# Kernel optimization log

Measured on AMD Instinct MI355X. Metric: run time of the kernel, lower is better.

The kernel has to match this reference:

```python
import math
import jax, jax.numpy as jnp
import numpy as np

B, D, K = 512, 512, 93431
S_SCALE = 64.0
MARGIN = 0.5
EPS = 0.1
COS_M = math.cos(MARGIN)
SIN_M = math.sin(MARGIN)
THRESHOLD = math.cos(math.pi - MARGIN)
MM = math.sin(math.pi - MARGIN) * MARGIN


def setup_inputs() -> dict:
    key = jax.random.key(0)
    k1, k2, k3 = jax.random.split(key, 3)
    x = jax.random.normal(k1, (B, D), dtype=jnp.float32)
    label = jax.random.randint(k2, (B,), 0, K, dtype=jnp.int64)
    kernel = jax.random.normal(k3, (D, K), dtype=jnp.float32) * 0.01
    t = jnp.zeros((1,), dtype=jnp.float32)
    return {"x": x, "label": label, "kernel": kernel, "t": t}


def reference(x, label, kernel, t):
    # L2-normalize embeddings (rows) and kernel (columns), cosine logits
    xn = x / jnp.linalg.norm(x, axis=1, keepdims=True)
    kn = kernel / jnp.linalg.norm(kernel, axis=0, keepdims=True)
    cos_theta = jnp.clip(xn @ kn, -1.0, 1.0)  # [B, K]

    rows = jnp.arange(B)
    target_logit = cos_theta[rows, label]  # [B]
    sin_theta = jnp.sqrt(1.0 - target_logit ** 2)
    cos_theta_m = target_logit * COS_M - sin_theta * SIN_M  # [B]

    mask = cos_theta > cos_theta_m[:, None]  # [B, K]
    final_target_logit = jnp.where(target_logit > THRESHOLD,
                                   cos_theta_m, target_logit - MM)

    # buffer update runs under no_grad in torch; updated t is used immediately
    t_new = jax.lax.stop_gradient(target_logit.mean() * 0.01 + 0.99 * t[0])

    # hard-example re-weighting, then scatter margin logit at the label column
    ct = jnp.where(mask, cos_theta * (t_new + cos_theta), cos_theta)
    ct = ct.at[rows, label].set(final_target_logit)
    logits = ct * S_SCALE

    # label-smoothed cross-entropy without materializing the one-hot matrix
    logp = jax.nn.log_softmax(logits, axis=1)  # [B, K]
    nll = (1.0 - EPS) * logp[rows, label] + (EPS / K) * logp.sum(axis=1)
    loss = -nll.mean()
    return loss
```

## Files before the change

### kernel.cpp

```cpp
#include <hip/hip_runtime.h>
#include <math.h>

#define BB 512
#define DD 512
#define KK 93431
#define KPAD 93440

#define S_SCALEf 64.0f
#define COS_Mf   0.87758256189037276f
#define SIN_Mf   0.47942553860420301f
#define THRESHf (-0.87758256189037276f)
#define MMf      0.23971276930210151f
#define EPSf     0.1f
#define MFIXf    65.0f

#define KSCALE 64.0f
#define XSCALE 16.0f
#define INV_KX (1.0f / (KSCALE * XSCALE))

typedef float f32x4 __attribute__((ext_vector_type(4)));
typedef long  l64x2 __attribute__((ext_vector_type(2)));

__device__ __forceinline__ unsigned pack4_fp8(float a, float b, float c, float d) {
    unsigned v = 0;
    v = __builtin_amdgcn_cvt_pk_fp8_f32(a, b, v, false);
    v = __builtin_amdgcn_cvt_pk_fp8_f32(c, d, v, true);
    return v;
}

__device__ __forceinline__ void gload16(const void* g, void* l) {
    __builtin_amdgcn_global_load_lds(
        (const __attribute__((address_space(1))) unsigned int*)g,
        (__attribute__((address_space(3))) unsigned int*)l, 16, 0, 0);
}

__global__ void rownorm_k(const float* __restrict__ x, float* __restrict__ xn,
                          unsigned char* __restrict__ xnf8) {
    int b = blockIdx.x;
    int t = threadIdx.x;
    float v0 = x[b * DD + t];
    float v1 = x[b * DD + t + 256];
    float ss = v0 * v0 + v1 * v1;
    for (int off = 32; off; off >>= 1) ss += __shfl_down(ss, off);
    __shared__ float wred[4];
    __shared__ float s_inv;
    __shared__ float rbF[512];
    if ((t & 63) == 0) wred[t >> 6] = ss;
    __syncthreads();
    if (t == 0) s_inv = rsqrtf(wred[0] + wred[1] + wred[2] + wred[3]);
    __syncthreads();
    float inv = s_inv;
    float a0 = v0 * inv, a1 = v1 * inv;
    xn[b * DD + t]       = a0;
    xn[b * DD + t + 256] = a1;
    rbF[t]       = a0;
    rbF[t + 256] = a1;
    __syncthreads();
    if (t < 64) {
        int kt = t >> 3, ch = t & 7;
        float v[8];
#pragma unroll
        for (int e = 0; e < 8; ++e) v[e] = XSCALE * rbF[kt * 64 + ch * 8 + e];
        unsigned w0 = pack4_fp8(v[0], v[1], v[2], v[3]);
        unsigned w1 = pack4_fp8(v[4], v[5], v[6], v[7]);
        uint2 o = {w0, w1};
        int off = (ch < 4) ? ch * 16 : (ch - 4) * 16 + 8;
        *reinterpret_cast<uint2*>(&xnf8[(size_t)b * DD + kt * 64 + off]) = o;
    }
}

__global__ __launch_bounds__(256) void tcvt_k(const float* __restrict__ ker,
                                              unsigned char* __restrict__ kerf8,
                                              float* __restrict__ ssq) {
    __shared__ float tile[64][65];
    __shared__ float sp[256];
    int t = threadIdx.x;
    int c0 = blockIdx.x * 64;
    int lc = t & 63;
    int dq = t >> 6;
    int gc = c0 + lc;
    bool valid = gc < KK;
    float ss = 0.f;

    for (int kt = 0; kt < 8; ++kt) {
        const int d0 = kt * 64;
        __syncthreads();
#pragma unroll
        for (int i = 0; i < 16; ++i) {
            int d = dq + i * 4;
            float v = valid ? ker[(size_t)(d0 + d) * KK + gc] : 0.f;
            tile[d][lc] = v;
            ss = fmaf(v, v, ss);
        }
        __syncthreads();
#pragma unroll
        for (int j = 0; j < 2; ++j) {
            int l = t + 256 * j;
            int c = l >> 3;
            int ch = l & 7;
            float v[8];
#pragma unroll
            for (int e = 0; e < 8; ++e) v[e] = KSCALE * tile[ch * 8 + e][c];
            unsigned w0 = pack4_fp8(v[0], v[1], v[2], v[3]);
            unsigned w1 = pack4_fp8(v[4], v[5], v[6], v[7]);
            uint2 o = {w0, w1};
            int off = (ch < 4) ? ch * 16 : (ch - 4) * 16 + 8;
            *reinterpret_cast<uint2*>(&kerf8[(size_t)(c0 + c) * DD + kt * 64 + off]) = o;
        }
    }
    sp[t] = ss;
    __syncthreads();
    if (t < 64) ssq[c0 + t] = sp[t] + sp[t + 64] + sp[t + 128] + sp[t + 192];
}

__global__ void target_k(const float* __restrict__ xn, const float* __restrict__ ker,
                         const float* __restrict__ ssq, const int* __restrict__ label,
                         float* __restrict__ tl) {
    int b = blockIdx.x;
    int lane = threadIdx.x;
    int col = label[b];
    float acc = 0.f;
#pragma unroll
    for (int d = lane; d < DD; d += 64)
        acc = fmaf(xn[b * DD + d], ker[(size_t)d * KK + col], acc);
    for (int off = 32; off; off >>= 1) acc += __shfl_down(acc, off);
    if (lane == 0) {
        float c = acc * rsqrtf(ssq[col]);
        c = fminf(1.f, fmaxf(-1.f, c));
        tl[b] = c;
    }
}

__global__ void scalar_k(const float* __restrict__ tl, const float* __restrict__ t_in,
                         float* __restrict__ ctm, float* __restrict__ ftl,
                         float* __restrict__ tnew, float* __restrict__ ssq,
                         float* __restrict__ gse, float* __restrict__ gsl) {
    int t = threadIdx.x;
    float v = tl[t];
    __shared__ float red[8];
    __shared__ float s_tn;
    float s = v;
    for (int off = 32; off; off >>= 1) s += __shfl_down(s, off);
    if ((t & 63) == 0) red[t >> 6] = s;
    __syncthreads();
    if (t == 0) {
        float tot = 0.f;
        for (int i = 0; i < 8; ++i) tot += red[i];
        s_tn = (tot / 512.0f) * 0.01f + 0.99f * t_in[0];
        tnew[0] = s_tn;
    }
    __syncthreads();
    float st = sqrtf(fmaxf(0.f, 1.f - v * v));
    float cm = v * COS_Mf - st * SIN_Mf;
    ctm[t] = cm;
    ftl[t] = (v > THRESHf) ? cm : (v - MMf);
    gse[t] = 0.f;
    gsl[t] = 0.f;
    if (t < KPAD - KK) ssq[KK + t] = 1.f;
}

#define TMt 128
#define TNt 128
#define NWG ((KPAD / TNt) * (BB / TMt))

__global__ __launch_bounds__(256, 4) void gemm_k(
    const unsigned char* __restrict__ xnf8,
    const unsigned char* __restrict__ kerf8,
    const float* __restrict__ ssq,
    const int* __restrict__ label,
    const float* __restrict__ ctm, const float* __restrict__ ftl,
    const float* __restrict__ tnew,
    float* __restrict__ gse, float* __restrict__ gsl)
{
    __shared__ __align__(16) unsigned char As[2][TMt * 64];
    __shared__ __align__(16) unsigned char Bs[2][TNt * 64];
    __shared__ float se_s[TMt], sl_s[TMt], ctm_s[TMt], ftl_s[TMt];
    __shared__ int   lbl_s[TMt];

    int wg = blockIdx.x;
    int id = (wg & 7) * (NWG / 8) + (wg >> 3);
    int by = id & 3;
    int bx = id >> 2;
    int row0 = by * TMt;
    int col0 = bx * TNt;

    const int t = threadIdx.x;
    const int lane = t & 63;
    const int w = t >> 6;
    const int wm = w >> 1;
    const int wn = w & 1;
    const int cp0 = lane & 15;
    const int kq = lane >> 4;

    if (t < TMt) {
        se_s[t] = 0.f; sl_s[t] = 0.f;
        int r = row0 + t;
        ctm_s[t] = ctm[r]; ftl_s[t] = ftl[r]; lbl_s[t] = label[r];
    }
    const float tn = tnew[0];

    float sq4[4];
#pragma unroll
    for (int fc = 0; fc < 4; ++fc)
        sq4[fc] = ssq[col0 + wn * 64 + fc * 16 + cp0];

#define STAGE(ktv, bi)                                                         \
    {                                                                          \
        _Pragma("unroll")                                                      \
        for (int j = 0; j < 2; ++j) {                                          \
            const int l = t + 256 * j;                                         \
            const int r = l >> 2, s = l & 3;                                   \
            const int ss2 = s ^ ((r >> 1) & 3);                                \
            gload16(&xnf8[(size_t)(row0 + r) * DD + (ktv) * 64 + ss2 * 16],    \
                    (void*)&As[bi][l * 16]);                                   \
        }                                                                      \
        _Pragma("unroll")                                                      \
        for (int j = 0; j < 2; ++j) {                                          \
            const int l = t + 256 * j;                                         \
            const int r = l >> 2, s = l & 3;                                   \
            const int ss2 = s ^ ((r >> 1) & 3);                                \
            gload16(&kerf8[(size_t)(col0 + r) * DD + (ktv) * 64 + ss2 * 16],   \
                    (void*)&Bs[bi][l * 16]);                                   \
        }                                                                      \
    }

    f32x4 acc[4][4];
#pragma unroll
    for (int fm = 0; fm < 4; ++fm)
#pragma unroll
        for (int fc = 0; fc < 4; ++fc) acc[fm][fc] = (f32x4)0.f;

    STAGE(0, 0);
    __builtin_amdgcn_sched_barrier(0);
    asm volatile("s_waitcnt vmcnt(0)" ::: "memory");
    __builtin_amdgcn_s_barrier();

#pragma unroll
    for (int kt = 0; kt < 8; ++kt) {
        const int bi = kt & 1;
        if (kt < 7) STAGE(kt + 1, bi ^ 1);
        const char* Ap = (const char*)&As[bi][0];
        const char* Bp = (const char*)&Bs[bi][0];

        l64x2 bv[4];
#pragma unroll
        for (int fc = 0; fc < 4; ++fc) {
            const int ct = wn * 64 + fc * 16 + cp0;
            bv[fc] = *reinterpret_cast<const l64x2*>(
                Bp + ct * 64 + ((kq ^ ((ct >> 1) & 3)) * 16));
        }
        __builtin_amdgcn_s_setprio(1);
#pragma unroll
        for (int fm = 0; fm < 4; ++fm) {
            const int rt = wm * 64 + fm * 16 + cp0;
            l64x2 av = *reinterpret_cast<const l64x2*>(
                Ap + rt * 64 + ((kq ^ ((rt >> 1) & 3)) * 16));
#pragma unroll
            for (int fc = 0; fc < 4; ++fc) {
                acc[fm][fc] = __builtin_amdgcn_mfma_f32_16x16x32_fp8_fp8(
                    av[0], bv[fc][0], acc[fm][fc], 0, 0, 0);
                acc[fm][fc] = __builtin_amdgcn_mfma_f32_16x16x32_fp8_fp8(
                    av[1], bv[fc][1], acc[fm][fc], 0, 0, 0);
            }
        }
        __builtin_amdgcn_s_setprio(0);

        __builtin_amdgcn_sched_barrier(0);
        asm volatile("s_waitcnt vmcnt(0)" ::: "memory");
        __builtin_amdgcn_s_barrier();
    }
#undef STAGE

    float inv4[4];
#pragma unroll
    for (int fc = 0; fc < 4; ++fc) inv4[fc] = rsqrtf(sq4[fc]) * INV_KX;

#pragma unroll
    for (int fm = 0; fm < 4; ++fm) {
#pragma unroll
        for (int reg = 0; reg < 4; ++reg) {
            const int rt = wm * 64 + fm * 16 + (kq << 2) + reg;
            float cm = ctm_s[rt], ft = ftl_s[rt];
            const int rel = lbl_s[rt] - (col0 + wn * 64 + cp0);
            float se = 0.f, sl = 0.f;
#pragma unroll
            for (int fc = 0; fc < 4; ++fc) {
                float c = acc[fm][fc][reg] * inv4[fc];
                c = fminf(1.f, fmaxf(-1.f, c));
                float v = (c > cm) ? c * (tn + c) : c;
                if (rel == fc * 16) v = ft;
                float lg = S_SCALEf * v;
                se += __expf(lg - MFIXf);
                sl += lg;
            }
#pragma unroll
            for (int off = 8; off; off >>= 1) {
                se += __shfl_down(se, off, 16);
                sl += __shfl_down(sl, off, 16);
            }
            if (cp0 == 0) {
                atomicAdd(&se_s[rt], se);
                atomicAdd(&sl_s[rt], sl);
            }
        }
    }
    __syncthreads();
    if (t < TMt) {
        atomicAdd(&gse[row0 + t], se_s[t]);
        atomicAdd(&gsl[row0 + t], sl_s[t]);
    }
}

__global__ void loss_k(const float* __restrict__ gse, const float* __restrict__ gsl,
                       const float* __restrict__ ftl, float* __restrict__ out) {
    int t = threadIdx.x;
    float lse = MFIXf + logf(gse[t]);
    float lbl_logit = S_SCALEf * ftl[t];
    float nll = (1.f - EPSf) * (lbl_logit - lse)
              + (EPSf / (float)KK) * (gsl[t] - (float)KK * lse);
    __shared__ float red[8];
    float s = nll;
    for (int off = 32; off; off >>= 1) s += __shfl_down(s, off);
    if ((t & 63) == 0) red[t >> 6] = s;
    __syncthreads();
    if (t == 0) {
        float tot = 0.f;
        for (int i = 0; i < 8; ++i) tot += red[i];
        out[0] = -(tot / 512.0f);
    }
}

extern "C" void kernel_launch(void* const* d_in, const int* in_sizes, int n_in,
                              void* d_out, int out_size, void* d_ws, size_t ws_size,
                              hipStream_t stream) {
    const float* x     = (const float*)d_in[0];
    const int*   label = (const int*)d_in[1];
    const float* ker   = (const float*)d_in[2];
    const float* t_in  = (const float*)d_in[3];
    float* out = (float*)d_out;

    float* ws   = (float*)d_ws;
    float* xn   = ws;
    float* ssq  = xn + 262144;
    float* gse  = ssq + KPAD;
    float* gsl  = gse + 512;
    float* tl   = gsl + 512;
    float* ctm  = tl + 512;
    float* ftl  = ctm + 512;
    float* tnew = ftl + 512;
    unsigned char* xnf8  = (unsigned char*)(tnew + 64);
    unsigned char* kerf8 = xnf8 + (size_t)512 * 512;

    rownorm_k<<<BB, 256, 0, stream>>>(x, xn, xnf8);
    tcvt_k<<<KPAD / 64, 256, 0, stream>>>(ker, kerf8, ssq);
    target_k<<<BB, 64, 0, stream>>>(xn, ker, ssq, label, tl);
    scalar_k<<<1, 512, 0, stream>>>(tl, t_in, ctm, ftl, tnew, ssq, gse, gsl);
    gemm_k<<<NWG, 256, 0, stream>>>(xnf8, kerf8, ssq, label, ctm, ftl, tnew, gse, gsl);
    loss_k<<<1, 512, 0, stream>>>(gse, gsl, ftl, out);
}
```

Before: 126.7 us.

## Make GEMM persistent with register-resident A fragments and striped kernel panels

The fused cosine-logit GEMM becomes a persistent grid of 512 workgroups of 512 threads. Each workgroup holds its 128 rows of fp8 embeddings in registers, preformatted into MFMA fragment order by rownorm_k, and streams 64-column kernel panels with full K depth through double-buffered LDS. Partial sums for the softmax and label-smoothing terms stay in registers across panels, so atomics happen once per workgroup instead of once per tile. This removes repeated A-tile loads and per-tile launch and atomic overhead. The cost is a smaller MFMA tile per wave (16x64), a barrier per panel, and higher register pressure.

```diff
diff --git a/kernel.cpp b/kernel.cpp
--- a/kernel.cpp
+++ b/kernel.cpp
@@ -35,7 +35,7 @@
 }
 
 __global__ void rownorm_k(const float* __restrict__ x, float* __restrict__ xn,
-                          unsigned char* __restrict__ xnf8) {
+                          unsigned char* __restrict__ xnf8f) {
     int b = blockIdx.x;
     int t = threadIdx.x;
     float v0 = x[b * DD + t];
@@ -56,16 +56,21 @@
     rbF[t]       = a0;
     rbF[t + 256] = a1;
     __syncthreads();
-    if (t < 64) {
-        int kt = t >> 3, ch = t & 7;
-        float v[8];
-#pragma unroll
-        for (int e = 0; e < 8; ++e) v[e] = XSCALE * rbF[kt * 64 + ch * 8 + e];
-        unsigned w0 = pack4_fp8(v[0], v[1], v[2], v[3]);
-        unsigned w1 = pack4_fp8(v[4], v[5], v[6], v[7]);
-        uint2 o = {w0, w1};
-        int off = (ch < 4) ? ch * 16 : (ch - 4) * 16 + 8;
-        *reinterpret_cast<uint2*>(&xnf8[(size_t)b * DD + kt * 64 + off]) = o;
+    if (t < 32) {
+        int kt64 = t >> 2, kq = t & 3;
+        const int lo = kt64 * 64 + kq * 8;
+        const int hi = kt64 * 64 + (kq + 4) * 8;
+        unsigned w0 = pack4_fp8(XSCALE * rbF[lo + 0], XSCALE * rbF[lo + 1],
+                                XSCALE * rbF[lo + 2], XSCALE * rbF[lo + 3]);
+        unsigned w1 = pack4_fp8(XSCALE * rbF[lo + 4], XSCALE * rbF[lo + 5],
+                                XSCALE * rbF[lo + 6], XSCALE * rbF[lo + 7]);
+        unsigned w2 = pack4_fp8(XSCALE * rbF[hi + 0], XSCALE * rbF[hi + 1],
+                                XSCALE * rbF[hi + 2], XSCALE * rbF[hi + 3]);
+        unsigned w3 = pack4_fp8(XSCALE * rbF[hi + 4], XSCALE * rbF[hi + 5],
+                                XSCALE * rbF[hi + 6], XSCALE * rbF[hi + 7]);
+        uint4 o = {w0, w1, w2, w3};
+        size_t ci = ((size_t)(b >> 4) * 8 + kt64) * 64 + (b & 15) + (kq << 4);
+        *reinterpret_cast<uint4*>(&xnf8f[ci * 16]) = o;
     }
 }
 
@@ -159,12 +164,11 @@
     if (t < KPAD - KK) ssq[KK + t] = 1.f;
 }
 
-#define TMt 128
-#define TNt 128
-#define NWG ((KPAD / TNt) * (BB / TMt))
-
-__global__ __launch_bounds__(256, 4) void gemm_k(
-    const unsigned char* __restrict__ xnf8,
+#define NPAN 1460
+#define NSTR 128
+
+__global__ __launch_bounds__(512, 4) void gemm_k(
+    const unsigned char* __restrict__ xnf8f,
     const unsigned char* __restrict__ kerf8,
     const float* __restrict__ ssq,
     const int* __restrict__ label,
@@ -172,120 +176,118 @@
     const float* __restrict__ tnew,
     float* __restrict__ gse, float* __restrict__ gsl)
 {
-    __shared__ __align__(16) unsigned char As[2][TMt * 64];
-    __shared__ __align__(16) unsigned char Bs[2][TNt * 64];
-    __shared__ float se_s[TMt], sl_s[TMt], ctm_s[TMt], ftl_s[TMt];
-    __shared__ int   lbl_s[TMt];
+    __shared__ __align__(16) unsigned char Bs[2][64 * 512];
+    __shared__ float ctm_s[128], ftl_s[128];
+    __shared__ int   lbl_s[128];
 
     int wg = blockIdx.x;
-    int id = (wg & 7) * (NWG / 8) + (wg >> 3);
-    int by = id & 3;
-    int bx = id >> 2;
-    int row0 = by * TMt;
-    int col0 = bx * TNt;
+    int id = (wg & 7) * 64 + (wg >> 3);
+    const int g = id & 3;
+    const int s = id >> 2;
+    const int row0 = g * 128;
 
     const int t = threadIdx.x;
     const int lane = t & 63;
     const int w = t >> 6;
-    const int wm = w >> 1;
-    const int wn = w & 1;
     const int cp0 = lane & 15;
     const int kq = lane >> 4;
 
-    if (t < TMt) {
-        se_s[t] = 0.f; sl_s[t] = 0.f;
+    if (t < 128) {
         int r = row0 + t;
         ctm_s[t] = ctm[r]; ftl_s[t] = ftl[r]; lbl_s[t] = label[r];
     }
     const float tn = tnew[0];
 
-    float sq4[4];
-#pragma unroll
-    for (int fc = 0; fc < 4; ++fc)
-        sq4[fc] = ssq[col0 + wn * 64 + fc * 16 + cp0];
-
-#define STAGE(ktv, bi)                                                         \
+    l64x2 a2[8];
+    {
+        const unsigned char* base =
+            xnf8f + (size_t)((g * 8 + w) * 8) * 64 * 16;
+#pragma unroll
+        for (int kt = 0; kt < 8; ++kt)
+            a2[kt] = *reinterpret_cast<const l64x2*>(
+                base + ((size_t)kt * 64 + lane) * 16);
+    }
+#pragma unroll
+    for (int kt = 0; kt < 8; ++kt)
+        asm volatile("" :: "v"(__builtin_bit_cast(f32x4, a2[kt])));
+    __builtin_amdgcn_sched_barrier(0);
+
+    const int np = (s < NPAN - 11 * NSTR) ? 12 : 11;
+
+#define STAGEB(pv, q)                                                          \
     {                                                                          \
+        const size_t pb = (size_t)(pv) * 64 * 512;                             \
         _Pragma("unroll")                                                      \
-        for (int j = 0; j < 2; ++j) {                                          \
-            const int l = t + 256 * j;                                         \
-            const int r = l >> 2, s = l & 3;                                   \
-            const int ss2 = s ^ ((r >> 1) & 3);                                \
-            gload16(&xnf8[(size_t)(row0 + r) * DD + (ktv) * 64 + ss2 * 16],    \
-                    (void*)&As[bi][l * 16]);                                   \
+        for (int j = 0; j < 4; ++j) {                                          \
+            const int l = t + 512 * j;                                         \
+            const int c = l >> 5, sl = l & 31;                                 \
+            const int ps = sl ^ (c & 31);                                      \
+            gload16(&kerf8[pb + (size_t)c * 512 + ps * 16],                    \
+                    (void*)&Bs[q][l * 16]);                                    \
         }                                                                      \
-        _Pragma("unroll")                                                      \
-        for (int j = 0; j < 2; ++j) {                                          \
-            const int l = t + 256 * j;                                         \
-            const int r = l >> 2, s = l & 3;                                   \
-            const int ss2 = s ^ ((r >> 1) & 3);                                \
-            gload16(&kerf8[(size_t)(col0 + r) * DD + (ktv) * 64 + ss2 * 16],   \
-                    (void*)&Bs[bi][l * 16]);                                   \
-        }                                                                      \
-    }
-
-    f32x4 acc[4][4];
-#pragma unroll
-    for (int fm = 0; fm < 4; ++fm)
-#pragma unroll
-        for (int fc = 0; fc < 4; ++fc) acc[fm][fc] = (f32x4)0.f;
-
-    STAGE(0, 0);
+    }
+
+    STAGEB(s, 0);
     __builtin_amdgcn_sched_barrier(0);
-    asm volatile("s_waitcnt vmcnt(0)" ::: "memory");
+    asm volatile("s_waitcnt vmcnt(0) lgkmcnt(0)" ::: "memory");
     __builtin_amdgcn_s_barrier();
 
-#pragma unroll
-    for (int kt = 0; kt < 8; ++kt) {
-        const int bi = kt & 1;
-        if (kt < 7) STAGE(kt + 1, bi ^ 1);
-        const char* Ap = (const char*)&As[bi][0];
-        const char* Bp = (const char*)&Bs[bi][0];
-
-        l64x2 bv[4];
-#pragma unroll
-        for (int fc = 0; fc < 4; ++fc) {
-            const int ct = wn * 64 + fc * 16 + cp0;
-            bv[fc] = *reinterpret_cast<const l64x2*>(
-                Bp + ct * 64 + ((kq ^ ((ct >> 1) & 3)) * 16));
-        }
+    float regse[4] = {0.f, 0.f, 0.f, 0.f};
+    float regsl[4] = {0.f, 0.f, 0.f, 0.f};
+
+    int buf = 0;
+    for (int pi = 0; pi < np; ++pi) {
+        const int p = s + pi * NSTR;
+        float sq4[4];
+#pragma unroll
+        for (int fc = 0; fc < 4; ++fc)
+            sq4[fc] = ssq[p * 64 + fc * 16 + cp0];
+        if (pi + 1 < np) {
+            STAGEB(p + NSTR, buf ^ 1);
+            __builtin_amdgcn_sched_barrier(0);
+            asm volatile("s_waitcnt vmcnt(4)" ::: "memory");
+        } else {
+            __builtin_amdgcn_sched_barrier(0);
+            asm volatile("s_waitcnt vmcnt(0)" ::: "memory");
+        }
+        __builtin_amdgcn_s_barrier();
+
+        f32x4 acc[4];
+#pragma unroll
+        for (int fc = 0; fc < 4; ++fc) acc[fc] = (f32x4)0.f;
+        const char* Bp = (const char*)&Bs[buf][0];
         __builtin_amdgcn_s_setprio(1);
 #pragma unroll
-        for (int fm = 0; fm < 4; ++fm) {
-            const int rt = wm * 64 + fm * 16 + cp0;
-            l64x2 av = *reinterpret_cast<const l64x2*>(
-                Ap + rt * 64 + ((kq ^ ((rt >> 1) & 3)) * 16));
+        for (int kt = 0; kt < 8; ++kt) {
+            l64x2 bv[4];
 #pragma unroll
             for (int fc = 0; fc < 4; ++fc) {
-                acc[fm][fc] = __builtin_amdgcn_mfma_f32_16x16x32_fp8_fp8(
-                    av[0], bv[fc][0], acc[fm][fc], 0, 0, 0);
-                acc[fm][fc] = __builtin_amdgcn_mfma_f32_16x16x32_fp8_fp8(
-                    av[1], bv[fc][1], acc[fm][fc], 0, 0, 0);
+                const int ct = fc * 16 + cp0;
+                const int slot = (kt * 4 + kq) ^ (ct & 31);
+                bv[fc] = *reinterpret_cast<const l64x2*>(Bp + ct * 512 + slot * 16);
             }
+#pragma unroll
+            for (int fc = 0; fc < 4; ++fc) {
+                acc[fc] = __builtin_amdgcn_mfma_f32_16x16x32_fp8_fp8(
+                    a2[kt][0], bv[fc][0], acc[fc], 0, 0, 0);
+                acc[fc] = __builtin_amdgcn_mfma_f32_16x16x32_fp8_fp8(
+                    a2[kt][1], bv[fc][1], acc[fc], 0, 0, 0);
+            }
         }
         __builtin_amdgcn_s_setprio(0);
 
-        __builtin_amdgcn_sched_barrier(0);
-        asm volatile("s_waitcnt vmcnt(0)" ::: "memory");
-        __builtin_amdgcn_s_barrier();
-    }
-#undef STAGE
-
-    float inv4[4];
-#pragma unroll
-    for (int fc = 0; fc < 4; ++fc) inv4[fc] = rsqrtf(sq4[fc]) * INV_KX;
-
-#pragma unroll
-    for (int fm = 0; fm < 4; ++fm) {
+        float inv4[4];
+#pragma unroll
+        for (int fc = 0; fc < 4; ++fc) inv4[fc] = rsqrtf(sq4[fc]) * INV_KX;
 #pragma unroll
         for (int reg = 0; reg < 4; ++reg) {
-            const int rt = wm * 64 + fm * 16 + (kq << 2) + reg;
+            const int rt = w * 16 + (kq << 2) + reg;
             float cm = ctm_s[rt], ft = ftl_s[rt];
-            const int rel = lbl_s[rt] - (col0 + wn * 64 + cp0);
+            const int rel = lbl_s[rt] - (p * 64 + cp0);
             float se = 0.f, sl = 0.f;
 #pragma unroll
             for (int fc = 0; fc < 4; ++fc) {
-                float c = acc[fm][fc][reg] * inv4[fc];
+                float c = acc[fc][reg] * inv4[fc];
                 c = fminf(1.f, fmaxf(-1.f, c));
                 float v = (c > cm) ? c * (tn + c) : c;
                 if (rel == fc * 16) v = ft;
@@ -293,21 +295,27 @@
                 se += __expf(lg - MFIXf);
                 sl += lg;
             }
-#pragma unroll
-            for (int off = 8; off; off >>= 1) {
-                se += __shfl_down(se, off, 16);
-                sl += __shfl_down(sl, off, 16);
-            }
-            if (cp0 == 0) {
-                atomicAdd(&se_s[rt], se);
-                atomicAdd(&sl_s[rt], sl);
-            }
-        }
-    }
-    __syncthreads();
-    if (t < TMt) {
-        atomicAdd(&gse[row0 + t], se_s[t]);
-        atomicAdd(&gsl[row0 + t], sl_s[t]);
+            regse[reg] += se;
+            regsl[reg] += sl;
+        }
+        __builtin_amdgcn_s_barrier();
+        buf ^= 1;
+    }
+#undef STAGEB
+
+#pragma unroll
+    for (int reg = 0; reg < 4; ++reg) {
+        float se = regse[reg], sl = regsl[reg];
+#pragma unroll
+        for (int off = 8; off; off >>= 1) {
+            se += __shfl_down(se, off, 16);
+            sl += __shfl_down(sl, off, 16);
+        }
+        if (cp0 == 0) {
+            const int row = row0 + w * 16 + (kq << 2) + reg;
+            atomicAdd(&gse[row], se);
+            atomicAdd(&gsl[row], sl);
+        }
     }
 }
 
@@ -348,13 +356,13 @@
     float* ctm  = tl + 512;
     float* ftl  = ctm + 512;
     float* tnew = ftl + 512;
-    unsigned char* xnf8  = (unsigned char*)(tnew + 64);
-    unsigned char* kerf8 = xnf8 + (size_t)512 * 512;
-
-    rownorm_k<<<BB, 256, 0, stream>>>(x, xn, xnf8);
+    unsigned char* xnf8f = (unsigned char*)(tnew + 64);
+    unsigned char* kerf8 = xnf8f + (size_t)512 * 512;
+
+    rownorm_k<<<BB, 256, 0, stream>>>(x, xn, xnf8f);
     tcvt_k<<<KPAD / 64, 256, 0, stream>>>(ker, kerf8, ssq);
     target_k<<<BB, 64, 0, stream>>>(xn, ker, ssq, label, tl);
     scalar_k<<<1, 512, 0, stream>>>(tl, t_in, ctm, ftl, tnew, ssq, gse, gsl);
-    gemm_k<<<NWG, 256, 0, stream>>>(xnf8, kerf8, ssq, label, ctm, ftl, tnew, gse, gsl);
+    gemm_k<<<512, 512, 0, stream>>>(xnf8f, kerf8, ssq, label, ctm, ftl, tnew, gse, gsl);
     loss_k<<<1, 512, 0, stream>>>(gse, gsl, ftl, out);
 }
```

Measured after the change: 121.8 us, median of 2. -3.9%, faster.
